# Optimization experiments

Hardware: AMD Instinct MI355X
Metric: run time of the kernel (lower is better)

## Reference

```python
import jax, jax.numpy as jnp
import numpy as np

WS = 7      # window_size
NH = 12     # num_heads
SHIFT = 3   # shift_size

def _rel_pos_index(ws):
    coords = np.stack(np.meshgrid(np.arange(ws), np.arange(ws), indexing='ij')).reshape(2, -1)
    rel = (coords[:, :, None] - coords[:, None, :]).transpose(1, 2, 0)  # [N,N,2]
    rel[..., 0] += ws - 1
    rel[..., 1] += ws - 1
    rel[..., 0] *= 2 * ws - 1
    return jnp.asarray(rel.sum(-1))  # [N,N] int

REL_IDX = _rel_pos_index(WS)

def _ln(x, g, b, eps=1e-5):
    m = x.mean(-1, keepdims=True)
    v = ((x - m) ** 2).mean(-1, keepdims=True)
    return (x - m) / jnp.sqrt(v + eps) * g + b

def setup_inputs() -> dict:
    key = jax.random.key(0)
    ks = jax.random.split(key, 10)
    B, H, W, C = 16, 56, 56, 384
    Dff = 4 * C
    s = 0.02
    return {
        'x': jax.random.normal(ks[0], (B, H * W, C), jnp.float32),
        'norm1_g': jnp.ones((C,), jnp.float32),
        'norm1_b': jnp.zeros((C,), jnp.float32),
        'qkv_w': jax.random.normal(ks[1], (3 * C, C), jnp.float32) * s,
        'qkv_b': jax.random.normal(ks[2], (3 * C,), jnp.float32) * s,
        'proj_w': jax.random.normal(ks[3], (C, C), jnp.float32) * s,
        'proj_b': jax.random.normal(ks[4], (C,), jnp.float32) * s,
        'rpb_table': jax.random.normal(ks[5], ((2 * WS - 1) ** 2, NH), jnp.float32) * s,
        'norm2_g': jnp.ones((C,), jnp.float32),
        'norm2_b': jnp.zeros((C,), jnp.float32),
        'mlp_w1': jax.random.normal(ks[6], (Dff, C), jnp.float32) * s,
        'mlp_b1': jax.random.normal(ks[7], (Dff,), jnp.float32) * s,
        'mlp_w2': jax.random.normal(ks[8], (C, Dff), jnp.float32) * s,
        'mlp_b2': jax.random.normal(ks[9], (C,), jnp.float32) * s,
        'H': H,
        'W': W,
    }

def reference(x, norm1_g, norm1_b, qkv_w, qkv_b, proj_w, proj_b, rpb_table,
              norm2_g, norm2_b, mlp_w1, mlp_b1, mlp_w2, mlp_b2, H, W):
    B, L, C = x.shape
    # --- norm1 + shift + window partition ---
    h = _ln(x, norm1_g, norm1_b).reshape(B, H, W, C)
    h = jnp.roll(h, (-SHIFT, -SHIFT), axis=(1, 2))
    nh, nw = H // WS, W // WS
    xw = h.reshape(B, nh, WS, nw, WS, C).transpose(0, 1, 3, 2, 4, 5).reshape(-1, WS * WS, C)
    # --- window attention with relative position bias ---
    Bw, N, _ = xw.shape
    hd = C // NH
    qkv = (xw @ qkv_w.T + qkv_b).reshape(Bw, N, 3, NH, hd).transpose(2, 0, 3, 1, 4)
    q, k, v = qkv[0] * (hd ** -0.5), qkv[1], qkv[2]  # [Bw,NH,N,hd]
    attn = jnp.einsum('bhnd,bhmd->bhnm', q, k)
    bias = rpb_table[REL_IDX.reshape(-1)].reshape(N, N, NH).transpose(2, 0, 1)  # [NH,N,N]
    attn = jax.nn.softmax(attn + bias[None], axis=-1)
    o = jnp.einsum('bhnm,bhmd->bhnd', attn, v).transpose(0, 2, 1, 3).reshape(Bw, N, C)
    o = o @ proj_w.T + proj_b
    # --- window reverse + unshift + residual ---
    o = o.reshape(B, nh, nw, WS, WS, C).transpose(0, 1, 3, 2, 4, 5).reshape(B, H, W, C)
    o = jnp.roll(o, (SHIFT, SHIFT), axis=(1, 2)).reshape(B, L, C)
    x = x + o
    # --- MLP ---
    h = _ln(x, norm2_g, norm2_b)
    h = jax.nn.gelu(h @ mlp_w1.T + mlp_b1, approximate=False) @ mlp_w2.T + mlp_b2
    return x + h
```

## Files before the change

### kernel.cpp

```cpp
#include <hip/hip_runtime.h>

typedef unsigned short ushort_t;
typedef unsigned int uint32;
typedef __attribute__((ext_vector_type(8))) short short8;
typedef __attribute__((ext_vector_type(4))) float floatx4;

static __device__ __forceinline__ ushort_t f2bf(float f) {
    union { float f; unsigned int u; } c; c.f = f;
    unsigned int u = c.u;
    return (ushort_t)((u + 0x7FFFu + ((u >> 16) & 1u)) >> 16);
}

static __device__ __forceinline__ int swz_off(int row, int slot16) {
    return row * 64 + (((slot16 ^ (row & 7)) & 7) << 3);
}

__global__ __launch_bounds__(256) void cvt_weights(
    const float* __restrict__ w0, const float* __restrict__ w1,
    const float* __restrict__ w2, const float* __restrict__ w3,
    ushort_t* __restrict__ o0, ushort_t* __restrict__ o1,
    ushort_t* __restrict__ o2, ushort_t* __restrict__ o3)
{
    int i = blockIdx.x * 256 + threadIdx.x;
    if (i < 442368) o0[i] = f2bf(w0[i]);
    if (i < 147456) o1[i] = f2bf(w1[i]);
    if (i < 589824) o2[i] = f2bf(w2[i]);
    if (i < 589824) o3[i] = f2bf(w3[i]);
}

__global__ __launch_bounds__(256) void build_bias(
    const float* __restrict__ rpb, float* __restrict__ biasT)
{
    int idx = blockIdx.x * 256 + threadIdx.x;
    int h = idx >> 12, j = (idx >> 6) & 63, q = idx & 63;
    float v = 0.f;
    if (q < 49 && j < 49) {
        int pi = q / 7, pj = q - pi * 7;
        int qi = j / 7, qj = j - qi * 7;
        v = rpb[((pi - qi + 6) * 13 + (pj - qj + 6)) * 12 + h];
    }
    biasT[idx] = v;
}

template<bool WPART>
__global__ __launch_bounds__(256) void ln_kernel(
    const float* __restrict__ x, const float* __restrict__ g,
    const float* __restrict__ b, ushort_t* __restrict__ out)
{
    int wave = threadIdx.x >> 6, lane = threadIdx.x & 63;
    int tkn = blockIdx.x * 4 + wave;
    const float* src;
    if (WPART) {
        int w = tkn / 49, n = tkn - w * 49;
        int bb = w >> 6, wrem = w & 63;
        int wi = wrem >> 3, wj = wrem & 7;
        int pi = n / 7, pj = n - pi * 7;
        int si = wi * 7 + pi + 3; if (si >= 56) si -= 56;
        int sj = wj * 7 + pj + 3; if (sj >= 56) sj -= 56;
        src = x + ((size_t)bb * 3136 + si * 56 + sj) * 384;
    } else {
        src = x + (size_t)tkn * 384;
    }
    float v[6];
    float s = 0.f, sq = 0.f;
#pragma unroll
    for (int it = 0; it < 3; ++it) {
        float2 t = *(const float2*)(src + it * 128 + lane * 2);
        v[it * 2] = t.x; v[it * 2 + 1] = t.y;
        s += t.x + t.y; sq += t.x * t.x + t.y * t.y;
    }
#pragma unroll
    for (int off = 32; off; off >>= 1) {
        s += __shfl_xor(s, off, 64);
        sq += __shfl_xor(sq, off, 64);
    }
    float mean = s * (1.f / 384.f);
    float rstd = rsqrtf(sq * (1.f / 384.f) - mean * mean + 1e-5f);
    ushort_t* dst = out + (size_t)tkn * 384;
#pragma unroll
    for (int it = 0; it < 3; ++it) {
        int c = it * 128 + lane * 2;
        float2 gg = *(const float2*)(g + c);
        float2 bb2 = *(const float2*)(b + c);
        float y0 = (v[it * 2] - mean) * rstd * gg.x + bb2.x;
        float y1 = (v[it * 2 + 1] - mean) * rstd * gg.y + bb2.y;
        uint32 pack = ((uint32)f2bf(y0)) | (((uint32)f2bf(y1)) << 16);
        *(uint32*)(dst + c) = pack;
    }
}

template<int EPI>
__global__ __launch_bounds__(256, 2) void gemm_bt(
    const ushort_t* __restrict__ A, const ushort_t* __restrict__ Bw,
    const float* __restrict__ bias, void* __restrict__ out,
    const float* __restrict__ resid, int M, int N, int K)
{
    __shared__ __align__(16) ushort_t As[2][128 * 64];
    __shared__ __align__(16) ushort_t Bs[2][128 * 64];
    int tid = threadIdx.x;

    int nwg = gridDim.x;
    int orig = blockIdx.x;
    int xcd = orig & 7, lid = orig >> 3;
    int q8 = nwg >> 3, r8 = nwg & 7;
    int swz = (xcd < r8 ? xcd * (q8 + 1) : r8 * (q8 + 1) + (xcd - r8) * q8) + lid;
    int bnT = N >> 7;
    int bm = swz / bnT, bn = swz - bm * bnT;

    int wv = tid >> 6, lane = tid & 63;
    int wr = wv >> 1, wc = wv & 1;
    int quad = lane >> 4, l15 = lane & 15;
    int r0 = tid >> 3, s0 = tid & 7;

    floatx4 acc[4][4];
#pragma unroll
    for (int mi = 0; mi < 4; ++mi)
#pragma unroll
        for (int ni = 0; ni < 4; ++ni)
            acc[mi][ni] = (floatx4){0.f, 0.f, 0.f, 0.f};

    const ushort_t* Ar0 = A + (size_t)(bm * 128 + r0) * K + s0 * 8;
    const ushort_t* Ar1 = Ar0 + (size_t)32 * K;
    const ushort_t* Ar2 = Ar0 + (size_t)64 * K;
    const ushort_t* Ar3 = Ar0 + (size_t)96 * K;
    const ushort_t* Br0 = Bw + (size_t)(bn * 128 + r0) * K + s0 * 8;
    const ushort_t* Br1 = Br0 + (size_t)32 * K;
    const ushort_t* Br2 = Br0 + (size_t)64 * K;
    const ushort_t* Br3 = Br0 + (size_t)96 * K;

    int w0 = swz_off(r0, s0), w1 = swz_off(r0 + 32, s0);
    int w2 = swz_off(r0 + 64, s0), w3 = swz_off(r0 + 96, s0);

#define GLOAD(a0,a1,a2,a3,b0,b1,b2,b3,k0) \
    a0 = *(const uint4*)(Ar0 + (k0)); a1 = *(const uint4*)(Ar1 + (k0)); \
    a2 = *(const uint4*)(Ar2 + (k0)); a3 = *(const uint4*)(Ar3 + (k0)); \
    b0 = *(const uint4*)(Br0 + (k0)); b1 = *(const uint4*)(Br1 + (k0)); \
    b2 = *(const uint4*)(Br2 + (k0)); b3 = *(const uint4*)(Br3 + (k0));

#define SWRITE(buf,a0,a1,a2,a3,b0,b1,b2,b3) \
    *(uint4*)&As[buf][w0] = a0; *(uint4*)&As[buf][w1] = a1; \
    *(uint4*)&As[buf][w2] = a2; *(uint4*)&As[buf][w3] = a3; \
    *(uint4*)&Bs[buf][w0] = b0; *(uint4*)&Bs[buf][w1] = b1; \
    *(uint4*)&Bs[buf][w2] = b2; *(uint4*)&Bs[buf][w3] = b3;

#define COMPUTE(buf) \
    _Pragma("unroll") \
    for (int kk = 0; kk < 64; kk += 32) { \
        short8 af[4], bfr[4]; \
        _Pragma("unroll") \
        for (int mi = 0; mi < 4; ++mi) \
            af[mi] = *(const short8*)&As[buf][swz_off(wr * 64 + mi * 16 + l15, (kk >> 3) + quad)]; \
        _Pragma("unroll") \
        for (int ni = 0; ni < 4; ++ni) \
            bfr[ni] = *(const short8*)&Bs[buf][swz_off(wc * 64 + ni * 16 + l15, (kk >> 3) + quad)]; \
        _Pragma("unroll") \
        for (int mi = 0; mi < 4; ++mi) \
            _Pragma("unroll") \
            for (int ni = 0; ni < 4; ++ni) \
                acc[mi][ni] = __builtin_amdgcn_mfma_f32_16x16x32_bf16( \
                    af[mi], bfr[ni], acc[mi][ni], 0, 0, 0); \
    }

    int nK = K >> 6;
    uint4 pa0, pa1, pa2, pa3, pb0, pb1, pb2, pb3;
    uint4 qa0, qa1, qa2, qa3, qb0, qb1, qb2, qb3;

    GLOAD(pa0, pa1, pa2, pa3, pb0, pb1, pb2, pb3, 0);
    GLOAD(qa0, qa1, qa2, qa3, qb0, qb1, qb2, qb3, 64);
    SWRITE(0, pa0, pa1, pa2, pa3, pb0, pb1, pb2, pb3);
    if (nK > 2) { GLOAD(pa0, pa1, pa2, pa3, pb0, pb1, pb2, pb3, 128); }
    __syncthreads();

    for (int kt = 0; kt < nK; kt += 2) {
        COMPUTE(0);
        SWRITE(1, qa0, qa1, qa2, qa3, qb0, qb1, qb2, qb3);
        if (kt + 3 < nK) { int k0 = (kt + 3) << 6; GLOAD(qa0, qa1, qa2, qa3, qb0, qb1, qb2, qb3, k0); }
        __syncthreads();
        COMPUTE(1);
        if (kt + 2 < nK) {
            SWRITE(0, pa0, pa1, pa2, pa3, pb0, pb1, pb2, pb3);
            if (kt + 4 < nK) { int k0 = (kt + 4) << 6; GLOAD(pa0, pa1, pa2, pa3, pb0, pb1, pb2, pb3, k0); }
            __syncthreads();
        }
    }
#undef GLOAD
#undef SWRITE
#undef COMPUTE

    if (EPI == 2) {
        float bv4[4];
#pragma unroll
        for (int ni = 0; ni < 4; ++ni) bv4[ni] = bias[bn * 128 + wc * 64 + ni * 16 + l15];
#pragma unroll
        for (int mi = 0; mi < 4; ++mi) {
#pragma unroll
            for (int r = 0; r < 4; ++r) {
                int gm = bm * 128 + wr * 64 + mi * 16 + quad * 4 + r;
                int wdx = gm / 49, n = gm - wdx * 49;
                int b = wdx >> 6, wrem = wdx & 63;
                int wi = wrem >> 3, wj = wrem & 7;
                int pi = n / 7, pj = n - pi * 7;
                int i = wi * 7 + pi + 3; if (i >= 56) i -= 56;
                int j = wj * 7 + pj + 3; if (j >= 56) j -= 56;
                size_t base = ((size_t)b * 3136 + i * 56 + j) * 384;
#pragma unroll
                for (int ni = 0; ni < 4; ++ni) {
                    size_t dst = base + bn * 128 + wc * 64 + ni * 16 + l15;
                    ((float*)out)[dst] = resid[dst] + acc[mi][ni][r] + bv4[ni];
                }
            }
        }
    } else {
#pragma unroll
        for (int mi = 0; mi < 4; ++mi) {
#pragma unroll
            for (int ni = 0; ni < 4; ++ni) {
                int gn = bn * 128 + wc * 64 + ni * 16 + l15;
                float bv = bias[gn];
#pragma unroll
                for (int r = 0; r < 4; ++r) {
                    int gm = bm * 128 + wr * 64 + mi * 16 + quad * 4 + r;
                    float v = acc[mi][ni][r] + bv;
                    if (EPI == 0) {
                        if (gn < 384) v *= 0.17677669529663689f;
                        ((ushort_t*)out)[(size_t)gm * N + gn] = f2bf(v);
                    } else if (EPI == 1) {
                        v = 0.5f * v * (1.f + erff(v * 0.70710678118654752f));
                        ((ushort_t*)out)[(size_t)gm * N + gn] = f2bf(v);
                    } else {
                        size_t dst = (size_t)gm * 384 + gn;
                        ((float*)out)[dst] = resid[dst] + v;
                    }
                }
            }
        }
    }
}

__global__ __launch_bounds__(256) void attn_kernel(
    const ushort_t* __restrict__ qkv,
    const float* __restrict__ biasT,
    ushort_t* __restrict__ O)
{
    __shared__ __align__(16) ushort_t Pl[4][64 * 64];
    int wave = threadIdx.x >> 6;
    int lane = threadIdx.x & 63;
    int id = blockIdx.x * 4 + wave;
    int w = id / 12, h = id % 12;
    int quad = lane >> 4, l15 = lane & 15;
    ushort_t* P = Pl[wave];

    short8 aQ[4], bK[4];
#pragma unroll
    for (int t = 0; t < 4; ++t) {
        int row = t * 16 + l15; if (row > 48) row = 48;
        aQ[t] = *(const short8*)(qkv + (size_t)(w * 49 + row) * 1152 + h * 32 + quad * 8);
        bK[t] = *(const short8*)(qkv + (size_t)(w * 49 + row) * 1152 + 384 + h * 32 + quad * 8);
    }
    floatx4 S[4][4];
    floatx4 z4 = (floatx4){0.f, 0.f, 0.f, 0.f};
#pragma unroll
    for (int mt = 0; mt < 4; ++mt)
#pragma unroll
        for (int nt = 0; nt < 4; ++nt)
            S[mt][nt] = __builtin_amdgcn_mfma_f32_16x16x32_bf16(aQ[mt], bK[nt], z4, 0, 0, 0);

    short8 aV[2][2];
#pragma unroll
    for (int mt = 0; mt < 2; ++mt)
#pragma unroll
        for (int kt = 0; kt < 2; ++kt) {
            short8 v;
#pragma unroll
            for (int t = 0; t < 8; ++t) {
                int j = kt * 32 + quad * 8 + t; if (j > 48) j = 48;
                v[t] = (short)qkv[(size_t)(w * 49 + j) * 1152 + 768 + h * 32 + mt * 16 + l15];
            }
            aV[mt][kt] = v;
        }

    const float* bT = biasT + h * 4096;
#pragma unroll
    for (int mt = 0; mt < 4; ++mt) {
        float4 bq[4];
#pragma unroll
        for (int nt = 0; nt < 4; ++nt)
            bq[nt] = *(const float4*)(bT + (nt * 16 + l15) * 64 + mt * 16 + quad * 4);
#pragma unroll
        for (int r = 0; r < 4; ++r) {
            int q = mt * 16 + quad * 4 + r;
            int key = (q ^ (q >> 3)) & 7;
            float mx = -1e30f;
#pragma unroll
            for (int nt = 0; nt < 4; ++nt) {
                int j = nt * 16 + l15;
                float sv = S[mt][nt][r] + ((const float*)&bq[nt])[r];
                if (j >= 49) sv = -1e30f;
                S[mt][nt][r] = sv;
                mx = fmaxf(mx, sv);
            }
#pragma unroll
            for (int off = 1; off < 16; off <<= 1) mx = fmaxf(mx, __shfl_xor(mx, off, 64));
            float sum = 0.f;
#pragma unroll
            for (int nt = 0; nt < 4; ++nt) {
                int j = nt * 16 + l15;
                float p = __expf(S[mt][nt][r] - mx);
                if (j >= 49) p = 0.f;
                S[mt][nt][r] = p;
                sum += p;
            }
#pragma unroll
            for (int off = 1; off < 16; off <<= 1) sum += __shfl_xor(sum, off, 64);
            float inv = 1.f / sum;
#pragma unroll
            for (int nt = 0; nt < 4; ++nt) {
                int j = nt * 16 + l15;
                P[q * 64 + (((j >> 3) ^ key) << 3) + (j & 7)] = f2bf(S[mt][nt][r] * inv);
            }
        }
    }
    asm volatile("s_waitcnt lgkmcnt(0)" ::: "memory");
    __builtin_amdgcn_sched_barrier(0);

    floatx4 Oc[2][4];
#pragma unroll
    for (int mt = 0; mt < 2; ++mt)
#pragma unroll
        for (int nt = 0; nt < 4; ++nt)
            Oc[mt][nt] = z4;
#pragma unroll
    for (int nt = 0; nt < 4; ++nt) {
        int query = nt * 16 + l15;
        int key = (query ^ (query >> 3)) & 7;
#pragma unroll
        for (int kt = 0; kt < 2; ++kt) {
            int slot = ((kt * 4 + quad) ^ key) & 7;
            short8 bP = *(const short8*)&P[query * 64 + slot * 8];
#pragma unroll
            for (int mt = 0; mt < 2; ++mt)
                Oc[mt][nt] = __builtin_amdgcn_mfma_f32_16x16x32_bf16(
                    aV[mt][kt], bP, Oc[mt][nt], 0, 0, 0);
        }
    }
#pragma unroll
    for (int nt = 0; nt < 4; ++nt) {
        int query = nt * 16 + l15;
        if (query < 49) {
#pragma unroll
            for (int mt = 0; mt < 2; ++mt) {
                ushort4 pk;
                pk.x = f2bf(Oc[mt][nt][0]);
                pk.y = f2bf(Oc[mt][nt][1]);
                pk.z = f2bf(Oc[mt][nt][2]);
                pk.w = f2bf(Oc[mt][nt][3]);
                *(ushort4*)(O + (size_t)(w * 49 + query) * 384 + h * 32 + mt * 16 + quad * 4) = pk;
            }
        }
    }
}

extern "C" void kernel_launch(void* const* d_in, const int* in_sizes, int n_in,
                              void* d_out, int out_size, void* d_ws, size_t ws_size,
                              hipStream_t stream) {
    const float* x      = (const float*)d_in[0];
    const float* n1g    = (const float*)d_in[1];
    const float* n1b    = (const float*)d_in[2];
    const float* qkv_w  = (const float*)d_in[3];
    const float* qkv_b  = (const float*)d_in[4];
    const float* proj_w = (const float*)d_in[5];
    const float* proj_b = (const float*)d_in[6];
    const float* rpb    = (const float*)d_in[7];
    const float* n2g    = (const float*)d_in[8];
    const float* n2b    = (const float*)d_in[9];
    const float* w1     = (const float*)d_in[10];
    const float* b1     = (const float*)d_in[11];
    const float* w2     = (const float*)d_in[12];
    const float* b2     = (const float*)d_in[13];
    float* out = (float*)d_out;
    char* ws = (char*)d_ws;

    ushort_t* qkvbuf = (ushort_t*)ws;
    ushort_t* bufA   = (ushort_t*)(ws + 115605504);
    ushort_t* wq     = (ushort_t*)(ws + 154140672);
    ushort_t* wp     = wq + 442368;
    ushort_t* wm1    = wp + 147456;
    ushort_t* wm2    = wm1 + 589824;
    float* biasT     = (float*)(ws + 154140672 + 3538944);

    cvt_weights<<<2304, 256, 0, stream>>>(qkv_w, proj_w, w1, w2, wq, wp, wm1, wm2);
    build_bias<<<192, 256, 0, stream>>>(rpb, biasT);

    ln_kernel<true><<<12544, 256, 0, stream>>>(x, n1g, n1b, bufA);
    gemm_bt<0><<<3528, 256, 0, stream>>>(bufA, wq, qkv_b, qkvbuf, nullptr, 50176, 1152, 384);
    attn_kernel<<<3072, 256, 0, stream>>>(qkvbuf, biasT, bufA);
    gemm_bt<2><<<1176, 256, 0, stream>>>(bufA, wp, proj_b, out, x, 50176, 384, 384);
    ln_kernel<false><<<12544, 256, 0, stream>>>(out, n2g, n2b, bufA);
    for (int half = 0; half < 2; ++half) {
        size_t mo = (size_t)half * 25088;
        gemm_bt<1><<<2352, 256, 0, stream>>>(bufA + mo * 384, wm1, b1, qkvbuf, nullptr, 25088, 1536, 384);
        gemm_bt<3><<<588, 256, 0, stream>>>(qkvbuf, wm2, b2, out + mo * 384, out + mo * 384, 25088, 384, 1536);
    }
}
```

Measured before the change: 562.3 us.

## Replace LDS-staged GEMM with direct global-to-register MFMA fragment loads

Removes shared-memory staging, swizzling and double buffering from the GEMM. Each wave now loads its MFMA fragments straight from global memory into registers, and K becomes a template parameter so the loop can be fully unrolled. This drops LDS traffic and barriers. In exchange, data is no longer shared between waves, so each A and B row is fetched by two waves and global and L2 traffic goes up. The loads are also 16-byte strided per lane, and latency hiding now relies on the compiler's scheduling.

```diff
diff --git a/kernel.cpp b/kernel.cpp
--- a/kernel.cpp
+++ b/kernel.cpp
@@ -9,10 +9,6 @@
     union { float f; unsigned int u; } c; c.f = f;
     unsigned int u = c.u;
     return (ushort_t)((u + 0x7FFFu + ((u >> 16) & 1u)) >> 16);
-}
-
-static __device__ __forceinline__ int swz_off(int row, int slot16) {
-    return row * 64 + (((slot16 ^ (row & 7)) & 7) << 3);
 }
 
 __global__ __launch_bounds__(256) void cvt_weights(
@@ -89,14 +85,12 @@
     }
 }
 
-template<int EPI>
-__global__ __launch_bounds__(256, 2) void gemm_bt(
+template<int EPI, int K>
+__global__ __launch_bounds__(256, 2) void gemm_rf(
     const ushort_t* __restrict__ A, const ushort_t* __restrict__ Bw,
     const float* __restrict__ bias, void* __restrict__ out,
-    const float* __restrict__ resid, int M, int N, int K)
-{
-    __shared__ __align__(16) ushort_t As[2][128 * 64];
-    __shared__ __align__(16) ushort_t Bs[2][128 * 64];
+    const float* __restrict__ resid, int M, int N)
+{
     int tid = threadIdx.x;
 
     int nwg = gridDim.x;
@@ -110,7 +104,6 @@
     int wv = tid >> 6, lane = tid & 63;
     int wr = wv >> 1, wc = wv & 1;
     int quad = lane >> 4, l15 = lane & 15;
-    int r0 = tid >> 3, s0 = tid & 7;
 
     floatx4 acc[4][4];
 #pragma unroll
@@ -119,73 +112,37 @@
         for (int ni = 0; ni < 4; ++ni)
             acc[mi][ni] = (floatx4){0.f, 0.f, 0.f, 0.f};
 
-    const ushort_t* Ar0 = A + (size_t)(bm * 128 + r0) * K + s0 * 8;
-    const ushort_t* Ar1 = Ar0 + (size_t)32 * K;
-    const ushort_t* Ar2 = Ar0 + (size_t)64 * K;
-    const ushort_t* Ar3 = Ar0 + (size_t)96 * K;
-    const ushort_t* Br0 = Bw + (size_t)(bn * 128 + r0) * K + s0 * 8;
-    const ushort_t* Br1 = Br0 + (size_t)32 * K;
-    const ushort_t* Br2 = Br0 + (size_t)64 * K;
-    const ushort_t* Br3 = Br0 + (size_t)96 * K;
-
-    int w0 = swz_off(r0, s0), w1 = swz_off(r0 + 32, s0);
-    int w2 = swz_off(r0 + 64, s0), w3 = swz_off(r0 + 96, s0);
-
-#define GLOAD(a0,a1,a2,a3,b0,b1,b2,b3,k0) \
-    a0 = *(const uint4*)(Ar0 + (k0)); a1 = *(const uint4*)(Ar1 + (k0)); \
-    a2 = *(const uint4*)(Ar2 + (k0)); a3 = *(const uint4*)(Ar3 + (k0)); \
-    b0 = *(const uint4*)(Br0 + (k0)); b1 = *(const uint4*)(Br1 + (k0)); \
-    b2 = *(const uint4*)(Br2 + (k0)); b3 = *(const uint4*)(Br3 + (k0));
-
-#define SWRITE(buf,a0,a1,a2,a3,b0,b1,b2,b3) \
-    *(uint4*)&As[buf][w0] = a0; *(uint4*)&As[buf][w1] = a1; \
-    *(uint4*)&As[buf][w2] = a2; *(uint4*)&As[buf][w3] = a3; \
-    *(uint4*)&Bs[buf][w0] = b0; *(uint4*)&Bs[buf][w1] = b1; \
-    *(uint4*)&Bs[buf][w2] = b2; *(uint4*)&Bs[buf][w3] = b3;
-
-#define COMPUTE(buf) \
-    _Pragma("unroll") \
-    for (int kk = 0; kk < 64; kk += 32) { \
-        short8 af[4], bfr[4]; \
-        _Pragma("unroll") \
-        for (int mi = 0; mi < 4; ++mi) \
-            af[mi] = *(const short8*)&As[buf][swz_off(wr * 64 + mi * 16 + l15, (kk >> 3) + quad)]; \
-        _Pragma("unroll") \
-        for (int ni = 0; ni < 4; ++ni) \
-            bfr[ni] = *(const short8*)&Bs[buf][swz_off(wc * 64 + ni * 16 + l15, (kk >> 3) + quad)]; \
-        _Pragma("unroll") \
-        for (int mi = 0; mi < 4; ++mi) \
-            _Pragma("unroll") \
-            for (int ni = 0; ni < 4; ++ni) \
-                acc[mi][ni] = __builtin_amdgcn_mfma_f32_16x16x32_bf16( \
-                    af[mi], bfr[ni], acc[mi][ni], 0, 0, 0); \
-    }
-
-    int nK = K >> 6;
-    uint4 pa0, pa1, pa2, pa3, pb0, pb1, pb2, pb3;
-    uint4 qa0, qa1, qa2, qa3, qb0, qb1, qb2, qb3;
-
-    GLOAD(pa0, pa1, pa2, pa3, pb0, pb1, pb2, pb3, 0);
-    GLOAD(qa0, qa1, qa2, qa3, qb0, qb1, qb2, qb3, 64);
-    SWRITE(0, pa0, pa1, pa2, pa3, pb0, pb1, pb2, pb3);
-    if (nK > 2) { GLOAD(pa0, pa1, pa2, pa3, pb0, pb1, pb2, pb3, 128); }
-    __syncthreads();
-
-    for (int kt = 0; kt < nK; kt += 2) {
-        COMPUTE(0);
-        SWRITE(1, qa0, qa1, qa2, qa3, qb0, qb1, qb2, qb3);
-        if (kt + 3 < nK) { int k0 = (kt + 3) << 6; GLOAD(qa0, qa1, qa2, qa3, qb0, qb1, qb2, qb3, k0); }
-        __syncthreads();
-        COMPUTE(1);
-        if (kt + 2 < nK) {
-            SWRITE(0, pa0, pa1, pa2, pa3, pb0, pb1, pb2, pb3);
-            if (kt + 4 < nK) { int k0 = (kt + 4) << 6; GLOAD(pa0, pa1, pa2, pa3, pb0, pb1, pb2, pb3, k0); }
-            __syncthreads();
-        }
-    }
-#undef GLOAD
-#undef SWRITE
-#undef COMPUTE
+    const ushort_t* Ab[4];
+    const ushort_t* Bb[4];
+#pragma unroll
+    for (int mi = 0; mi < 4; ++mi)
+        Ab[mi] = A + (size_t)(bm * 128 + wr * 64 + mi * 16 + l15) * K + quad * 8;
+#pragma unroll
+    for (int ni = 0; ni < 4; ++ni)
+        Bb[ni] = Bw + (size_t)(bn * 128 + wc * 64 + ni * 16 + l15) * K + quad * 8;
+
+#pragma unroll
+    for (int kt = 0; kt < K / 64; ++kt) {
+        short8 af[4][2], bf[4][2];
+#pragma unroll
+        for (int mi = 0; mi < 4; ++mi) {
+            af[mi][0] = *(const short8*)(Ab[mi] + kt * 64);
+            af[mi][1] = *(const short8*)(Ab[mi] + kt * 64 + 32);
+        }
+#pragma unroll
+        for (int ni = 0; ni < 4; ++ni) {
+            bf[ni][0] = *(const short8*)(Bb[ni] + kt * 64);
+            bf[ni][1] = *(const short8*)(Bb[ni] + kt * 64 + 32);
+        }
+#pragma unroll
+        for (int kh = 0; kh < 2; ++kh)
+#pragma unroll
+            for (int mi = 0; mi < 4; ++mi)
+#pragma unroll
+                for (int ni = 0; ni < 4; ++ni)
+                    acc[mi][ni] = __builtin_amdgcn_mfma_f32_16x16x32_bf16(
+                        af[mi][kh], bf[ni][kh], acc[mi][ni], 0, 0, 0);
+    }
 
     if (EPI == 2) {
         float bv4[4];
@@ -392,13 +349,13 @@
     build_bias<<<192, 256, 0, stream>>>(rpb, biasT);
 
     ln_kernel<true><<<12544, 256, 0, stream>>>(x, n1g, n1b, bufA);
-    gemm_bt<0><<<3528, 256, 0, stream>>>(bufA, wq, qkv_b, qkvbuf, nullptr, 50176, 1152, 384);
+    gemm_rf<0, 384><<<3528, 256, 0, stream>>>(bufA, wq, qkv_b, qkvbuf, nullptr, 50176, 1152);
     attn_kernel<<<3072, 256, 0, stream>>>(qkvbuf, biasT, bufA);
-    gemm_bt<2><<<1176, 256, 0, stream>>>(bufA, wp, proj_b, out, x, 50176, 384, 384);
+    gemm_rf<2, 384><<<1176, 256, 0, stream>>>(bufA, wp, proj_b, out, x, 50176, 384);
     ln_kernel<false><<<12544, 256, 0, stream>>>(out, n2g, n2b, bufA);
     for (int half = 0; half < 2; ++half) {
         size_t mo = (size_t)half * 25088;
-        gemm_bt<1><<<2352, 256, 0, stream>>>(bufA + mo * 384, wm1, b1, qkvbuf, nullptr, 25088, 1536, 384);
-        gemm_bt<3><<<588, 256, 0, stream>>>(qkvbuf, wm2, b2, out + mo * 384, out + mo * 384, 25088, 384, 1536);
-    }
-}
+        gemm_rf<1, 384><<<2352, 256, 0, stream>>>(bufA + mo * 384, wm1, b1, qkvbuf, nullptr, 25088, 1536);
+        gemm_rf<3, 1536><<<588, 256, 0, stream>>>(qkvbuf, wm2, b2, out + mo * 384, out + mo * 384, 25088, 384);
+    }
+}
```

After: 1.009 ms. 1.79x slower.
